# Optimization experiments

Hardware: AMD Instinct MI355X
Metric: run time of the kernel (lower is better)

Reference implementation:

```python
import jax, jax.numpy as jnp
import numpy as np
from jax.ops import segment_sum, segment_max

DIM = 64; EDGE_DIM = 6; ACTION_DIM = 6
N = 16384; E = 32768; G = 256; TPG = 12  # nodes, edges, graphs, torsions/graph


def setup_inputs() -> dict:
    key = jax.random.key(0)
    ks = jax.random.split(key, 16)
    d = DIM
    def lin(k, fo, fi):
        return (jax.random.normal(k, (fo, fi), jnp.float32) / np.sqrt(fi)).astype(jnp.float32)
    return {
        "x": jax.random.normal(ks[0], (N, 3), jnp.float32),
        "edge_attr": jax.random.normal(ks[1], (E, EDGE_DIM), jnp.float32),
        "edge_index": jax.random.randint(ks[2], (2, E), 0, N),
        "batch": (jnp.arange(N) // (N // G)).astype(jnp.int32),
        "nonring": jax.random.randint(ks[3], (G * TPG, 4), 0, N),
        "nrbidx": (jnp.arange(G * TPG) // TPG).astype(jnp.int32),
        "num_graphs": G,
        "torsion_size": TPG,
        "lin0_w": lin(ks[4], d, 3), "lin0_b": jnp.zeros((d,), jnp.float32),
        "e1_w": lin(ks[5], d, EDGE_DIM), "e1_b": jnp.zeros((d,), jnp.float32),
        "e2_w": lin(ks[6], d * d, d), "e2_b": jnp.zeros((d * d,), jnp.float32),
        "root_w": lin(ks[7], d, d), "conv_b": jnp.zeros((d,), jnp.float32),
        "gru_wih": lin(ks[8], 3 * d, d), "gru_whh": lin(ks[9], 3 * d, d),
        "gru_bih": jnp.zeros((3 * d,), jnp.float32), "gru_bhh": jnp.zeros((3 * d,), jnp.float32),
        "s2s_wih": lin(ks[10], 4 * d, 2 * d), "s2s_whh": lin(ks[11], 4 * d, d),
        "s2s_bih": jnp.zeros((4 * d,), jnp.float32), "s2s_bhh": jnp.zeros((4 * d,), jnp.float32),
        "mem_wih": lin(ks[12], 4 * d, 2 * d), "mem_whh": lin(ks[13], 4 * d, d),
        "mem_bih": jnp.zeros((4 * d,), jnp.float32), "mem_bhh": jnp.zeros((4 * d,), jnp.float32),
        "lin1_w": lin(ks[14], d, 5 * d), "lin1_b": jnp.zeros((d,), jnp.float32),
        "lin2_w": lin(ks[15], ACTION_DIM, d), "lin2_b": jnp.zeros((ACTION_DIM,), jnp.float32),
    }


def _lstm_step(xin, h, c, wih, whh, bih, bhh):
    g = xin @ wih.T + bih + h @ whh.T + bhh
    i, f, gg, o = jnp.split(g, 4, axis=-1)
    c = jax.nn.sigmoid(f) * c + jax.nn.sigmoid(i) * jnp.tanh(gg)
    h = jax.nn.sigmoid(o) * jnp.tanh(c)
    return h, c


def _model(x, edge_attr, lin0_w, lin0_b, e1_w, e1_b, e2_w, e2_b, root_w, conv_b,
           gru_wih, gru_whh, gru_bih, gru_bhh, s2s_wih, s2s_whh, s2s_bih, s2s_bhh,
           mem_wih, mem_whh, mem_bih, mem_bhh, lin1_w, lin1_b, lin2_w, lin2_b,
           edge_index, batch, nonring, nrbidx, num_graphs, torsion_size):
    d = lin0_w.shape[0]
    n = x.shape[0]
    out = jax.nn.relu(x @ lin0_w.T + lin0_b)           # [N, d]
    h = out                                            # GRU hidden
    src, dst = edge_index[0], edge_index[1]
    # edge-conditioned weights (fixed across the 6 iterations -> computed once)
    ew = (jax.nn.relu(edge_attr @ e1_w.T + e1_b) @ e2_w.T + e2_b).reshape(-1, d, d)  # [E, d, d]
    deg = jnp.clip(segment_sum(jnp.ones((src.shape[0],), out.dtype), dst, num_segments=n), 1.0)
    for _ in range(6):
        msg = jnp.einsum('ei,eio->eo', out[src], ew)   # per-edge matmul, [E, d]
        agg = segment_sum(msg, dst, num_segments=n) / deg[:, None]  # scatter-mean
        m = jax.nn.relu(agg + out @ root_w + conv_b)
        gi = m @ gru_wih.T + gru_bih
        gh = h @ gru_whh.T + gru_bhh
        r = jax.nn.sigmoid(gi[:, :d] + gh[:, :d])
        z = jax.nn.sigmoid(gi[:, d:2 * d] + gh[:, d:2 * d])
        nnew = jnp.tanh(gi[:, 2 * d:] + r * gh[:, 2 * d:])
        h = (1.0 - z) * nnew + z * h
        out = h
    # Set2Set pooling, 6 processing steps
    q_star = jnp.zeros((num_graphs, 2 * d), out.dtype)
    hs = jnp.zeros((num_graphs, d), out.dtype); cs = jnp.zeros_like(hs)
    for _ in range(6):
        hs, cs = _lstm_step(q_star, hs, cs, s2s_wih, s2s_whh, s2s_bih, s2s_bhh)
        e = jnp.sum(out * hs[batch], axis=-1)
        emax = segment_max(e, batch, num_segments=num_graphs)
        a = jnp.exp(e - emax[batch])
        a = a / segment_sum(a, batch, num_segments=num_graphs)[batch]
        r_ = segment_sum(a[:, None] * out, batch, num_segments=num_graphs)
        q_star = jnp.concatenate([hs, r_], axis=-1)
    # memory LSTM, single step from zero state
    hx = jnp.zeros((num_graphs, d), out.dtype); cx = jnp.zeros_like(hx)
    hx, cx = _lstm_step(q_star, hx, cx, mem_wih, mem_whh, mem_bih, mem_bhh)
    lstm_sel = hx[nrbidx]                                   # [T, d]
    node_sel = out[nonring.reshape(-1)].reshape(4, -1, d)   # faithful to .view(4,-1,dim)
    stacked = jnp.concatenate([lstm_sel[None], node_sel], axis=0)  # [5, T, d]
    feat = jnp.transpose(stacked, (2, 1, 0)).reshape(-1, 5 * d)    # faithful permute+reshape -> [T, 5d]
    o1 = jax.nn.relu(feat @ lin1_w.T + lin1_b)
    logits = o1 @ lin2_w.T + lin2_b                          # [T, action_dim]
    logit = logits.reshape(num_graphs, torsion_size, -1)     # uniform split + pad_sequence
    return logit, hx[None], cx[None]


def reference(x, edge_attr, edge_index, batch, nonring, nrbidx, num_graphs, torsion_size,
              lin0_w, lin0_b, e1_w, e1_b, e2_w, e2_b, root_w, conv_b,
              gru_wih, gru_whh, gru_bih, gru_bhh, s2s_wih, s2s_whh, s2s_bih, s2s_bhh,
              mem_wih, mem_whh, mem_bih, mem_bhh, lin1_w, lin1_b, lin2_w, lin2_b):
    return _model(x, edge_attr, lin0_w, lin0_b, e1_w, e1_b, e2_w, e2_b, root_w, conv_b,
                  gru_wih, gru_whh, gru_bih, gru_bhh, s2s_wih, s2s_whh, s2s_bih, s2s_bhh,
                  mem_wih, mem_whh, mem_bih, mem_bhh, lin1_w, lin1_b, lin2_w, lin2_b,
                  edge_index, batch, nonring, nrbidx, num_graphs, torsion_size)
```

## Files before the change

kernel.cpp:

```cpp
#include <hip/hip_runtime.h>

#define NNODE 16384
#define NEDGE 32768
#define NG    256
#define TPGx  12
#define TTOT  (NG * TPGx)
#define D     64

typedef _Float16 h8 __attribute__((ext_vector_type(8)));
typedef float    f4 __attribute__((ext_vector_type(4)));

static __device__ __forceinline__ float sigm(float x) { return 1.f / (1.f + __expf(-x)); }

static __device__ __forceinline__ f4 mfma16h(h8 a, h8 b, f4 c) {
  return __builtin_amdgcn_mfma_f32_16x16x32_f16(a, b, c, 0, 0, 0);
}

static __device__ __forceinline__ void gload_lds16(const void* g, void* l) {
  __builtin_amdgcn_global_load_lds(
      (const __attribute__((address_space(1))) unsigned int*)g,
      (__attribute__((address_space(3))) unsigned int*)l, 16, 0, 0);
}

#define WS_H      0
#define WS_AGG    4194304
#define WS_W2     8388608
#define WS_RT     8921088
#define WS_WHH    8929280
#define WS_WIH    8953856
#define WS_SWIH   8978432
#define WS_SWHH   9109504
#define WS_MWIH   9175040
#define WS_L1WF   9306112
#define WS_L2WF   9388032
#define WS_FB     9389568
#define WS_DEG    9398784
#define WS_HX     9464320
#define WS_NEED   9529856

struct Srcs { const void* p[23]; };

__device__ __constant__ const int kCum[24] = {
    0, 192, 256, 640, 704, 262848, 266944, 271040, 271104, 283392, 295680,
    295872, 296064, 328832, 345216, 345472, 345728, 378496, 378752, 379008,
    399488, 399552, 399936, 399942};

__global__ __launch_bounds__(256) void pack_kernel(Srcs S, char* __restrict__ ws) {
  int idx = blockIdx.x * 256 + threadIdx.x;
  if (idx >= 399942) return;
  int r = 0, base = 0;
#pragma unroll
  for (int k = 0; k < 23; k++)
    if (idx >= kCum[k]) { r = k; base = kCum[k]; }
  int li = idx - base;
  float v = ((const float*)S.p[r])[li];

  float*    fb   = (float*)(ws + WS_FB);
  _Float16* w2   = (_Float16*)(ws + WS_W2);
  _Float16* rtH  = (_Float16*)(ws + WS_RT);
  _Float16* whhH = (_Float16*)(ws + WS_WHH);
  _Float16* wihH = (_Float16*)(ws + WS_WIH);
  float*    swih = (float*)(ws + WS_SWIH);
  float*    swhh = (float*)(ws + WS_SWHH);
  float*    mwih = (float*)(ws + WS_MWIH);
  float*    l1w  = (float*)(ws + WS_L1WF);
  float*    l2w  = (float*)(ws + WS_L2WF);

  switch (r) {
    case 0: fb[li] = v; break;
    case 1: fb[192 + li] = v; break;
    case 2: fb[256 + li] = v; break;
    case 3: fb[640 + li] = v; break;
    case 4: {
      int i = li >> 12, o = (li >> 6) & 63, k = li & 63;
      w2[i * 4096 + (((k >> 3) * 64 + o) << 3) + (k & 7)] = (_Float16)v;
    } break;
    case 5: {
      int k = li >> 6, o = li & 63;
      w2[64 * 4096 + (((k >> 3) * 64 + o) << 3) + (k & 7)] = (_Float16)v;
    } break;
    case 6: {
      int i = li >> 6, o = li & 63;
      rtH[o * 64 + i] = (_Float16)v;
    } break;
    case 7: fb[704 + li] = v; break;
    case 8: wihH[li] = (_Float16)v; break;
    case 9: whhH[li] = (_Float16)v; break;
    case 10: fb[768 + li] = v; break;
    case 11: fb[960 + li] = v; break;
    case 12: swih[li] = v; break;
    case 13: swhh[li] = v; break;
    case 14: fb[1152 + li] = v; break;
    case 15: fb[1408 + li] = v; break;
    case 16: mwih[li] = v; break;
    case 17: fb[1664 + li] = v; break;
    case 18: fb[1920 + li] = v; break;
    case 19: l1w[li] = v; break;
    case 20: fb[2176 + li] = v; break;
    case 21: l2w[li] = v; break;
    case 22: fb[2240 + li] = v; break;
  }
}

__global__ __launch_bounds__(256) void init_kernel(
    const float* __restrict__ x, const float* __restrict__ fb,
    float* __restrict__ h) {
  int idx = blockIdx.x * 256 + threadIdx.x;
  int n = idx >> 6, o = idx & 63;
  float acc = fb[192 + o];
#pragma unroll
  for (int j = 0; j < 3; j++) acc += x[n * 3 + j] * fb[o * 3 + j];
  h[idx] = fmaxf(acc, 0.f);
}

__global__ __launch_bounds__(256) void deg_kernel(const int* __restrict__ edge_index,
                                                  float* __restrict__ deg) {
  int e = blockIdx.x * 256 + threadIdx.x;
  if (e < NEDGE) atomicAdd(&deg[edge_index[NEDGE + e]], 1.0f);
}

__global__ __launch_bounds__(256) void msg_kernel(
    const float* __restrict__ h, const float* __restrict__ ea,
    const float* __restrict__ fb, const _Float16* __restrict__ w2,
    const int* __restrict__ edge_index, float* __restrict__ agg) {
  __shared__ _Float16 sOut[64][72];
  __shared__ _Float16 sB[2][16384];
  const int tid = threadIdx.x;
  const int wave = tid >> 6, lane = tid & 63;
  const int m15 = lane & 15, quad = lane >> 4;
  const int eb = blockIdx.x * 64;
  {
    int r = tid >> 2, c0 = (tid & 3) * 16;
    int srcn = edge_index[eb + r];
#pragma unroll
    for (int c = c0; c < c0 + 16; c += 4) {
      float4 v = *(const float4*)&h[srcn * D + c];
      sOut[r][c]     = (_Float16)v.x;
      sOut[r][c + 1] = (_Float16)v.y;
      sOut[r][c + 2] = (_Float16)v.z;
      sOut[r][c + 3] = (_Float16)v.w;
    }
  }
  const int erow = wave * 16 + m15;
  const int e = eb + erow;
  float hid0[8], hid1[8];
  {
    float eav[6];
#pragma unroll
    for (int j = 0; j < 6; j++) eav[j] = ea[e * 6 + j];
#pragma unroll
    for (int j = 0; j < 8; j++) {
      int k0 = quad * 8 + j, k1 = 32 + quad * 8 + j;
      float a0 = fb[640 + k0], a1 = fb[640 + k1];
#pragma unroll
      for (int jj = 0; jj < 6; jj++) {
        a0 += eav[jj] * fb[256 + k0 * 6 + jj];
        a1 += eav[jj] * fb[256 + k1 * 6 + jj];
      }
      hid0[j] = fmaxf(a0, 0.f);
      hid1[j] = fmaxf(a1, 0.f);
    }
  }
  for (int c = wave; c < 32; c += 4)
    gload_lds16(w2 + c * 512 + lane * 8, &sB[0][c * 512]);
  __syncthreads();
  f4 zz = {0.f, 0.f, 0.f, 0.f};
  f4 acc0 = zz, acc1 = zz, acc2 = zz, acc3 = zz;
  for (int p = 0; p < 17; p++) {
    const int cur = p & 1;
    if (p < 16) {
      int nch = (p == 15) ? 8 : 32;
      const _Float16* src = w2 + (p + 1) * 4 * 4096;
      for (int c = wave; c < nch; c += 4)
        gload_lds16(src + c * 512 + lane * 8, &sB[cur ^ 1][c * 512]);
    }
    const int cnt = (p == 16) ? 1 : 4;
    for (int t = 0; t < cnt; t++) {
      const int i = p * 4 + t;
      h8 a0, a1;
      if (i < 64) {
        float os = (float)sOut[erow][i];
#pragma unroll
        for (int j = 0; j < 8; j++) {
          a0[j] = (_Float16)(os * hid0[j]);
          a1[j] = (_Float16)(os * hid1[j]);
        }
      } else {
#pragma unroll
        for (int j = 0; j < 8; j++) {
          a0[j] = sOut[erow][quad * 8 + j];
          a1[j] = sOut[erow][32 + quad * 8 + j];
        }
      }
      const _Float16* base = &sB[cur][t * 4096];
      const int q512 = quad * 512;
#pragma unroll
      for (int nt = 0; nt < 4; nt++) {
        int br8 = (nt * 16 + m15) * 8;
        h8 bh0 = *(const h8*)(base + q512 + br8);
        h8 bh1 = *(const h8*)(base + 2048 + q512 + br8);
        f4 a = (nt == 0) ? acc0 : (nt == 1) ? acc1 : (nt == 2) ? acc2 : acc3;
        a = mfma16h(a0, bh0, a);
        a = mfma16h(a1, bh1, a);
        if (nt == 0) acc0 = a; else if (nt == 1) acc1 = a; else if (nt == 2) acc2 = a; else acc3 = a;
      }
    }
    __syncthreads();
  }
#pragma unroll
  for (int reg = 0; reg < 4; reg++) {
    int ee = eb + wave * 16 + quad * 4 + reg;
    int dn = edge_index[NEDGE + ee];
    float* ap = agg + dn * D;
    atomicAdd(ap + m15,      acc0[reg]);
    atomicAdd(ap + 16 + m15, acc1[reg]);
    atomicAdd(ap + 32 + m15, acc2[reg]);
    atomicAdd(ap + 48 + m15, acc3[reg]);
  }
}

__global__ __launch_bounds__(256) void update_kernel(
    float* __restrict__ h, float* __restrict__ agg, const float* __restrict__ deg,
    const _Float16* __restrict__ rtH, const _Float16* __restrict__ whhH,
    const _Float16* __restrict__ wihH, const float* __restrict__ fb) {
  __shared__ float buf[64][68];
  const int tid = threadIdx.x;
  const int wave = tid >> 6, lane = tid & 63;
  const int m15 = lane & 15, quad = lane >> 4;
  const int nb = blockIdx.x * 64;
  {
    int r = tid >> 2, c0 = (tid & 3) * 16;
#pragma unroll
    for (int c = c0; c < c0 + 16; c += 4)
      *(float4*)&buf[r][c] = *(const float4*)&h[(nb + r) * D + c];
  }
  __syncthreads();
  const int mrow = wave * 16 + m15;
  h8 a0, a1;
#pragma unroll
  for (int j = 0; j < 8; j++) {
    a0[j] = (_Float16)buf[mrow][quad * 8 + j];
    a1[j] = (_Float16)buf[mrow][32 + quad * 8 + j];
  }
  f4 zz = {0.f, 0.f, 0.f, 0.f};
  f4 acc[16];
#pragma unroll
  for (int nt = 0; nt < 16; nt++) acc[nt] = zz;
#pragma unroll
  for (int nt = 0; nt < 16; nt++) {
    int nn = nt * 16 + m15;
    const _Float16* bp = (nt < 4) ? (rtH + nn * D) : (whhH + (nn - 64) * D);
    h8 bh0 = *(const h8*)(bp + quad * 8);
    h8 bh1 = *(const h8*)(bp + 32 + quad * 8);
    f4 a = acc[nt];
    a = mfma16h(a0, bh0, a);
    a = mfma16h(a1, bh1, a);
    acc[nt] = a;
  }
  __syncthreads();
#pragma unroll
  for (int nt = 0; nt < 4; nt++) {
#pragma unroll
    for (int reg = 0; reg < 4; reg++) {
      int nloc = wave * 16 + quad * 4 + reg;
      int o = nt * 16 + m15;
      float dg = fmaxf(deg[nb + nloc], 1.f);
      int aidx = (nb + nloc) * D + o;
      float v = acc[nt][reg] + agg[aidx] / dg + fb[704 + o];
      agg[aidx] = 0.f;
      buf[nloc][o] = fmaxf(v, 0.f);
    }
  }
  __syncthreads();
  h8 m0, m1;
#pragma unroll
  for (int j = 0; j < 8; j++) {
    m0[j] = (_Float16)buf[mrow][quad * 8 + j];
    m1[j] = (_Float16)buf[mrow][32 + quad * 8 + j];
  }
  f4 g2[12];
#pragma unroll
  for (int nt = 0; nt < 12; nt++) g2[nt] = zz;
#pragma unroll
  for (int nt = 0; nt < 12; nt++) {
    int nn = nt * 16 + m15;
    const _Float16* bp = wihH + nn * D;
    h8 bh0 = *(const h8*)(bp + quad * 8);
    h8 bh1 = *(const h8*)(bp + 32 + quad * 8);
    f4 a = g2[nt];
    a = mfma16h(m0, bh0, a);
    a = mfma16h(m1, bh1, a);
    g2[nt] = a;
  }
#pragma unroll
  for (int nt = 0; nt < 4; nt++) {
#pragma unroll
    for (int reg = 0; reg < 4; reg++) {
      int nloc = wave * 16 + quad * 4 + reg;
      int o = nt * 16 + m15;
      int gidx = (nb + nloc) * D + o;
      float gir = g2[nt][reg]      + fb[768 + o];
      float giz = g2[nt + 4][reg]  + fb[768 + 64 + o];
      float gin = g2[nt + 8][reg]  + fb[768 + 128 + o];
      float ghr = acc[nt + 4][reg]  + fb[960 + o];
      float ghz = acc[nt + 8][reg]  + fb[960 + 64 + o];
      float ghn = acc[nt + 12][reg] + fb[960 + 128 + o];
      float rr = sigm(gir + ghr);
      float zg = sigm(giz + ghz);
      float nnv = tanhf(gin + rr * ghn);
      float hv = h[gidx];
      h[gidx] = (1.f - zg) * nnv + zg * hv;
    }
  }
}

__global__ __launch_bounds__(256) void s2s_kernel(
    const float* __restrict__ h,
    const float* __restrict__ wih, const float* __restrict__ whhp,
    const float* __restrict__ mwih, const float* __restrict__ fb,
    float* __restrict__ hx_f32, float* __restrict__ dout) {
  __shared__ float outL[64][65];
  __shared__ float qs[128];
  __shared__ float hsv[64], csv[64], sg[256], sa[64];
  __shared__ float spart[4][64];
  const int t = threadIdx.x;
  const int g = blockIdx.x;
  for (int idx = t; idx < 64 * 64; idx += 256) outL[idx >> 6][idx & 63] = h[g * 4096 + idx];
  if (t < 128) qs[t] = 0.f;
  if (t < 64) { hsv[t] = 0.f; csv[t] = 0.f; }
  __syncthreads();
  for (int step = 0; step < 6; step++) {
    float acc = fb[1152 + t] + fb[1408 + t];
    const float* wr = wih + t * 128;
#pragma unroll 8
    for (int j = 0; j < 128; j++) acc += qs[j] * wr[j];
    const float* wr2 = whhp + t * 64;
#pragma unroll 8
    for (int j = 0; j < 64; j++) acc += hsv[j] * wr2[j];
    sg[t] = acc;
    __syncthreads();
    if (t < 64) {
      float cn = sigm(sg[64 + t]) * csv[t] + sigm(sg[t]) * tanhf(sg[128 + t]);
      csv[t] = cn;
      hsv[t] = sigm(sg[192 + t]) * tanhf(cn);
    }
    __syncthreads();
    if (t < 64) {
      float e = 0.f;
      for (int d2 = 0; d2 < 64; d2++) e += outL[t][d2] * hsv[d2];
      float mx = e;
      for (int off = 32; off > 0; off >>= 1) mx = fmaxf(mx, __shfl_xor(mx, off));
      float a = __expf(e - mx);
      float s = a;
      for (int off = 32; off > 0; off >>= 1) s += __shfl_xor(s, off);
      sa[t] = a / s;
    }
    __syncthreads();
    {
      int o = t & 63, part = t >> 6;
      float r = 0.f;
      for (int n2 = part * 16; n2 < part * 16 + 16; n2++) r += sa[n2] * outL[n2][o];
      spart[part][o] = r;
    }
    __syncthreads();
    if (t < 64) {
      qs[t] = hsv[t];
      qs[64 + t] = spart[0][t] + spart[1][t] + spart[2][t] + spart[3][t];
    }
    __syncthreads();
  }
  float acc = fb[1664 + t] + fb[1920 + t];
  const float* wr = mwih + t * 128;
#pragma unroll 8
  for (int j = 0; j < 128; j++) acc += qs[j] * wr[j];
  sg[t] = acc;
  __syncthreads();
  if (t < 64) {
    float cn = sigm(sg[t]) * tanhf(sg[128 + t]);
    float hn = sigm(sg[192 + t]) * tanhf(cn);
    hx_f32[g * 64 + t] = hn;
    dout[TTOT * 6 + g * 64 + t] = hn;
    dout[TTOT * 6 + NG * 64 + g * 64 + t] = cn;
  }
}

__global__ __launch_bounds__(64) void head_kernel(
    const float* __restrict__ h, const float* __restrict__ hx_f32,
    const int* __restrict__ nonring, const int* __restrict__ nrbidx,
    const float* __restrict__ l1w, const float* __restrict__ l2w,
    const float* __restrict__ fb, float* __restrict__ dout) {
  __shared__ float feat[320];
  __shared__ float so1[64];
  const int r = blockIdx.x;
  const int lane = threadIdx.x;
  const int blk = r % 48, di = r / 48;
  const int tt = blk * 64 + lane;
  feat[lane * 5] = hx_f32[nrbidx[tt] * 64 + di];
#pragma unroll
  for (int s = 1; s <= 4; s++)
    feat[lane * 5 + s] = h[nonring[(s - 1) * TTOT + tt] * 64 + di];
  __syncthreads();
  float acc = fb[2176 + lane];
  const float* wr = l1w + lane * 320;
#pragma unroll 8
  for (int c = 0; c < 320; c++) acc += feat[c] * wr[c];
  so1[lane] = fmaxf(acc, 0.f);
  __syncthreads();
  if (lane < 6) {
    float a2 = fb[2240 + lane];
    for (int j = 0; j < 64; j++) a2 += so1[j] * l2w[lane * 64 + j];
    dout[r * 6 + lane] = a2;
  }
}

extern "C" void kernel_launch(void* const* d_in, const int* in_sizes, int n_in,
                              void* d_out, int out_size, void* d_ws, size_t ws_size,
                              hipStream_t stream) {
  (void)in_sizes; (void)n_in; (void)out_size;
  const float* x         = (const float*)d_in[0];
  const float* edge_attr = (const float*)d_in[1];
  const int* edge_index  = (const int*)d_in[2];
  const int* nonring     = (const int*)d_in[4];
  const int* nrbidx      = (const int*)d_in[5];
  float* out = (float*)d_out;

  char* ws = (char*)d_ws;
  float*    h      = (float*)(ws + WS_H);
  float*    agg    = (float*)(ws + WS_AGG);
  _Float16* w2     = (_Float16*)(ws + WS_W2);
  _Float16* rtH    = (_Float16*)(ws + WS_RT);
  _Float16* whhH   = (_Float16*)(ws + WS_WHH);
  _Float16* wihH   = (_Float16*)(ws + WS_WIH);
  float*    swihF  = (float*)(ws + WS_SWIH);
  float*    swhhF  = (float*)(ws + WS_SWHH);
  float*    mwihF  = (float*)(ws + WS_MWIH);
  float*    l1wF   = (float*)(ws + WS_L1WF);
  float*    l2wF   = (float*)(ws + WS_L2WF);
  float*    fb     = (float*)(ws + WS_FB);
  float*    deg    = (float*)(ws + WS_DEG);
  float*    hx_f32 = (float*)(ws + WS_HX);
  if (ws_size < (size_t)WS_NEED) return;

  Srcs S;
  S.p[0] = d_in[8];   S.p[1] = d_in[9];   S.p[2] = d_in[10];  S.p[3] = d_in[11];
  S.p[4] = d_in[12];  S.p[5] = d_in[13];  S.p[6] = d_in[14];  S.p[7] = d_in[15];
  S.p[8] = d_in[16];  S.p[9] = d_in[17];  S.p[10] = d_in[18]; S.p[11] = d_in[19];
  S.p[12] = d_in[20]; S.p[13] = d_in[21]; S.p[14] = d_in[22]; S.p[15] = d_in[23];
  S.p[16] = d_in[24]; S.p[17] = d_in[26]; S.p[18] = d_in[27]; S.p[19] = d_in[28];
  S.p[20] = d_in[29]; S.p[21] = d_in[30]; S.p[22] = d_in[31];
  pack_kernel<<<(399942 + 255) / 256, 256, 0, stream>>>(S, ws);

  init_kernel<<<NNODE * D / 256, 256, 0, stream>>>(x, fb, h);
  hipMemsetAsync(deg, 0, NNODE * 4, stream);
  hipMemsetAsync(agg, 0, NNODE * D * 4, stream);
  deg_kernel<<<NEDGE / 256, 256, 0, stream>>>(edge_index, deg);

  for (int it = 0; it < 6; it++) {
    msg_kernel<<<NEDGE / 64, 256, 0, stream>>>(h, edge_attr, fb, w2, edge_index, agg);
    update_kernel<<<NNODE / 64, 256, 0, stream>>>(h, agg, deg, rtH, whhH, wihH, fb);
  }

  s2s_kernel<<<NG, 256, 0, stream>>>(h, swihF, swhhF, mwihF, fb, hx_f32, out);
  head_kernel<<<TTOT, 64, 0, stream>>>(h, hx_f32, nonring, nrbidx, l1wF, l2wF, fb, out);
}
```

Measured before the change: 540.0 us.

## Double msg_kernel edge tile, halve weight staging, transpose s2s/head weights

msg_kernel now handles 128 edges per block instead of 64. Each wave runs two 16-edge row tiles against the same B fragment loaded from LDS, which halves global-to-LDS traffic for the 64x64x64 edge-network weight per edge. The A operand is now built with packed fp16 vector multiplies on a precomputed fp16 hidden vector instead of a scalar fp32 loop. Separately, the s2s LSTM and head lin1 weights are packed transposed so that threads read them with coalesced loads. In exchange, msg_kernel uses more accumulator registers, launches half as many blocks, and rounds the hidden activations to fp16 before multiplying, which slightly changes numerics.

```diff
diff --git a/kernel.cpp b/kernel.cpp
--- a/kernel.cpp
+++ b/kernel.cpp
@@ -16,6 +16,11 @@
   return __builtin_amdgcn_mfma_f32_16x16x32_f16(a, b, c, 0, 0, 0);
 }
 
+static __device__ __forceinline__ h8 splat16(_Float16 x) {
+  h8 v = {x, x, x, x, x, x, x, x};
+  return v;
+}
+
 static __device__ __forceinline__ void gload_lds16(const void* g, void* l) {
   __builtin_amdgcn_global_load_lds(
       (const __attribute__((address_space(1))) unsigned int*)g,
@@ -28,10 +33,10 @@
 #define WS_RT     8921088
 #define WS_WHH    8929280
 #define WS_WIH    8953856
-#define WS_SWIH   8978432
-#define WS_SWHH   9109504
-#define WS_MWIH   9175040
-#define WS_L1WF   9306112
+#define WS_SWIHT  8978432
+#define WS_SWHHT  9109504
+#define WS_MWIHT  9175040
+#define WS_L1WT   9306112
 #define WS_L2WF   9388032
 #define WS_FB     9389568
 #define WS_DEG    9398784
@@ -55,16 +60,16 @@
   int li = idx - base;
   float v = ((const float*)S.p[r])[li];
 
-  float*    fb   = (float*)(ws + WS_FB);
-  _Float16* w2   = (_Float16*)(ws + WS_W2);
-  _Float16* rtH  = (_Float16*)(ws + WS_RT);
-  _Float16* whhH = (_Float16*)(ws + WS_WHH);
-  _Float16* wihH = (_Float16*)(ws + WS_WIH);
-  float*    swih = (float*)(ws + WS_SWIH);
-  float*    swhh = (float*)(ws + WS_SWHH);
-  float*    mwih = (float*)(ws + WS_MWIH);
-  float*    l1w  = (float*)(ws + WS_L1WF);
-  float*    l2w  = (float*)(ws + WS_L2WF);
+  float*    fb    = (float*)(ws + WS_FB);
+  _Float16* w2    = (_Float16*)(ws + WS_W2);
+  _Float16* rtH   = (_Float16*)(ws + WS_RT);
+  _Float16* whhH  = (_Float16*)(ws + WS_WHH);
+  _Float16* wihH  = (_Float16*)(ws + WS_WIH);
+  float*    swihT = (float*)(ws + WS_SWIHT);
+  float*    swhhT = (float*)(ws + WS_SWHHT);
+  float*    mwihT = (float*)(ws + WS_MWIHT);
+  float*    l1wT  = (float*)(ws + WS_L1WT);
+  float*    l2w   = (float*)(ws + WS_L2WF);
 
   switch (r) {
     case 0: fb[li] = v; break;
@@ -88,14 +93,14 @@
     case 9: whhH[li] = (_Float16)v; break;
     case 10: fb[768 + li] = v; break;
     case 11: fb[960 + li] = v; break;
-    case 12: swih[li] = v; break;
-    case 13: swhh[li] = v; break;
+    case 12: swihT[(li & 127) * 256 + (li >> 7)] = v; break;
+    case 13: swhhT[(li & 63) * 256 + (li >> 6)] = v; break;
     case 14: fb[1152 + li] = v; break;
     case 15: fb[1408 + li] = v; break;
-    case 16: mwih[li] = v; break;
+    case 16: mwihT[(li & 127) * 256 + (li >> 7)] = v; break;
     case 17: fb[1664 + li] = v; break;
     case 18: fb[1920 + li] = v; break;
-    case 19: l1w[li] = v; break;
+    case 19: l1wT[(li % 320) * 64 + (li / 320)] = v; break;
     case 20: fb[2176 + li] = v; break;
     case 21: l2w[li] = v; break;
     case 22: fb[2240 + li] = v; break;
@@ -123,17 +128,17 @@
     const float* __restrict__ h, const float* __restrict__ ea,
     const float* __restrict__ fb, const _Float16* __restrict__ w2,
     const int* __restrict__ edge_index, float* __restrict__ agg) {
-  __shared__ _Float16 sOut[64][72];
-  __shared__ _Float16 sB[2][16384];
+  __shared__ _Float16 sOut[128][72];
+  __shared__ _Float16 sB[2][8192];
   const int tid = threadIdx.x;
   const int wave = tid >> 6, lane = tid & 63;
   const int m15 = lane & 15, quad = lane >> 4;
-  const int eb = blockIdx.x * 64;
+  const int eb = blockIdx.x * 128;
   {
-    int r = tid >> 2, c0 = (tid & 3) * 16;
+    int r = tid >> 1, c0 = (tid & 1) * 32;
     int srcn = edge_index[eb + r];
 #pragma unroll
-    for (int c = c0; c < c0 + 16; c += 4) {
+    for (int c = c0; c < c0 + 32; c += 4) {
       float4 v = *(const float4*)&h[srcn * D + c];
       sOut[r][c]     = (_Float16)v.x;
       sOut[r][c + 1] = (_Float16)v.y;
@@ -141,56 +146,60 @@
       sOut[r][c + 3] = (_Float16)v.w;
     }
   }
-  const int erow = wave * 16 + m15;
-  const int e = eb + erow;
-  float hid0[8], hid1[8];
+  const int erow1 = wave * 16 + m15;
+  const int erow2 = 64 + erow1;
+  const int e1 = eb + erow1, e2 = eb + erow2;
+  h8 hidA0, hidA1, hidB0, hidB1;
   {
-    float eav[6];
-#pragma unroll
-    for (int j = 0; j < 6; j++) eav[j] = ea[e * 6 + j];
+    float eav1[6], eav2[6];
+#pragma unroll
+    for (int j = 0; j < 6; j++) { eav1[j] = ea[e1 * 6 + j]; eav2[j] = ea[e2 * 6 + j]; }
 #pragma unroll
     for (int j = 0; j < 8; j++) {
       int k0 = quad * 8 + j, k1 = 32 + quad * 8 + j;
-      float a0 = fb[640 + k0], a1 = fb[640 + k1];
+      float a01 = fb[640 + k0], a11 = fb[640 + k1];
+      float a02 = a01, a12 = a11;
 #pragma unroll
       for (int jj = 0; jj < 6; jj++) {
-        a0 += eav[jj] * fb[256 + k0 * 6 + jj];
-        a1 += eav[jj] * fb[256 + k1 * 6 + jj];
+        float w0 = fb[256 + k0 * 6 + jj], w1 = fb[256 + k1 * 6 + jj];
+        a01 += eav1[jj] * w0; a11 += eav1[jj] * w1;
+        a02 += eav2[jj] * w0; a12 += eav2[jj] * w1;
       }
-      hid0[j] = fmaxf(a0, 0.f);
-      hid1[j] = fmaxf(a1, 0.f);
-    }
-  }
-  for (int c = wave; c < 32; c += 4)
+      hidA0[j] = (_Float16)fmaxf(a01, 0.f);
+      hidA1[j] = (_Float16)fmaxf(a11, 0.f);
+      hidB0[j] = (_Float16)fmaxf(a02, 0.f);
+      hidB1[j] = (_Float16)fmaxf(a12, 0.f);
+    }
+  }
+  for (int c = wave; c < 16; c += 4)
     gload_lds16(w2 + c * 512 + lane * 8, &sB[0][c * 512]);
   __syncthreads();
   f4 zz = {0.f, 0.f, 0.f, 0.f};
-  f4 acc0 = zz, acc1 = zz, acc2 = zz, acc3 = zz;
-  for (int p = 0; p < 17; p++) {
+  f4 accA[4], accB[4];
+#pragma unroll
+  for (int nt = 0; nt < 4; nt++) { accA[nt] = zz; accB[nt] = zz; }
+  for (int p = 0; p < 33; p++) {
     const int cur = p & 1;
-    if (p < 16) {
-      int nch = (p == 15) ? 8 : 32;
-      const _Float16* src = w2 + (p + 1) * 4 * 4096;
+    if (p < 32) {
+      int nch = (p == 31) ? 8 : 16;
+      const _Float16* src = w2 + (p + 1) * 8192;
       for (int c = wave; c < nch; c += 4)
         gload_lds16(src + c * 512 + lane * 8, &sB[cur ^ 1][c * 512]);
     }
-    const int cnt = (p == 16) ? 1 : 4;
+    const int cnt = (p == 32) ? 1 : 2;
     for (int t = 0; t < cnt; t++) {
-      const int i = p * 4 + t;
-      h8 a0, a1;
+      const int i = p * 2 + t;
+      h8 a10, a11, a20, a21;
       if (i < 64) {
-        float os = (float)sOut[erow][i];
-#pragma unroll
-        for (int j = 0; j < 8; j++) {
-          a0[j] = (_Float16)(os * hid0[j]);
-          a1[j] = (_Float16)(os * hid1[j]);
-        }
+        h8 o1 = splat16(sOut[erow1][i]);
+        h8 o2 = splat16(sOut[erow2][i]);
+        a10 = hidA0 * o1; a11 = hidA1 * o1;
+        a20 = hidB0 * o2; a21 = hidB1 * o2;
       } else {
-#pragma unroll
-        for (int j = 0; j < 8; j++) {
-          a0[j] = sOut[erow][quad * 8 + j];
-          a1[j] = sOut[erow][32 + quad * 8 + j];
-        }
+        a10 = *(const h8*)&sOut[erow1][quad * 8];
+        a11 = *(const h8*)&sOut[erow1][32 + quad * 8];
+        a20 = *(const h8*)&sOut[erow2][quad * 8];
+        a21 = *(const h8*)&sOut[erow2][32 + quad * 8];
       }
       const _Float16* base = &sB[cur][t * 4096];
       const int q512 = quad * 512;
@@ -199,23 +208,27 @@
         int br8 = (nt * 16 + m15) * 8;
         h8 bh0 = *(const h8*)(base + q512 + br8);
         h8 bh1 = *(const h8*)(base + 2048 + q512 + br8);
-        f4 a = (nt == 0) ? acc0 : (nt == 1) ? acc1 : (nt == 2) ? acc2 : acc3;
-        a = mfma16h(a0, bh0, a);
-        a = mfma16h(a1, bh1, a);
-        if (nt == 0) acc0 = a; else if (nt == 1) acc1 = a; else if (nt == 2) acc2 = a; else acc3 = a;
+        accA[nt] = mfma16h(a10, bh0, accA[nt]);
+        accA[nt] = mfma16h(a11, bh1, accA[nt]);
+        accB[nt] = mfma16h(a20, bh0, accB[nt]);
+        accB[nt] = mfma16h(a21, bh1, accB[nt]);
       }
     }
     __syncthreads();
   }
 #pragma unroll
   for (int reg = 0; reg < 4; reg++) {
-    int ee = eb + wave * 16 + quad * 4 + reg;
-    int dn = edge_index[NEDGE + ee];
-    float* ap = agg + dn * D;
-    atomicAdd(ap + m15,      acc0[reg]);
-    atomicAdd(ap + 16 + m15, acc1[reg]);
-    atomicAdd(ap + 32 + m15, acc2[reg]);
-    atomicAdd(ap + 48 + m15, acc3[reg]);
+    int r1 = eb + wave * 16 + quad * 4 + reg;
+    int r2 = r1 + 64;
+    int dn1 = edge_index[NEDGE + r1];
+    int dn2 = edge_index[NEDGE + r2];
+    float* ap1 = agg + dn1 * D;
+    float* ap2 = agg + dn2 * D;
+#pragma unroll
+    for (int nt = 0; nt < 4; nt++) {
+      atomicAdd(ap1 + nt * 16 + m15, accA[nt][reg]);
+      atomicAdd(ap2 + nt * 16 + m15, accB[nt][reg]);
+    }
   }
 }
 
@@ -316,8 +329,8 @@
 
 __global__ __launch_bounds__(256) void s2s_kernel(
     const float* __restrict__ h,
-    const float* __restrict__ wih, const float* __restrict__ whhp,
-    const float* __restrict__ mwih, const float* __restrict__ fb,
+    const float* __restrict__ wihT, const float* __restrict__ whhT,
+    const float* __restrict__ mwihT, const float* __restrict__ fb,
     float* __restrict__ hx_f32, float* __restrict__ dout) {
   __shared__ float outL[64][65];
   __shared__ float qs[128];
@@ -331,12 +344,10 @@
   __syncthreads();
   for (int step = 0; step < 6; step++) {
     float acc = fb[1152 + t] + fb[1408 + t];
-    const float* wr = wih + t * 128;
 #pragma unroll 8
-    for (int j = 0; j < 128; j++) acc += qs[j] * wr[j];
-    const float* wr2 = whhp + t * 64;
+    for (int j = 0; j < 128; j++) acc += qs[j] * wihT[j * 256 + t];
 #pragma unroll 8
-    for (int j = 0; j < 64; j++) acc += hsv[j] * wr2[j];
+    for (int j = 0; j < 64; j++) acc += hsv[j] * whhT[j * 256 + t];
     sg[t] = acc;
     __syncthreads();
     if (t < 64) {
@@ -370,9 +381,8 @@
     __syncthreads();
   }
   float acc = fb[1664 + t] + fb[1920 + t];
-  const float* wr = mwih + t * 128;
 #pragma unroll 8
-  for (int j = 0; j < 128; j++) acc += qs[j] * wr[j];
+  for (int j = 0; j < 128; j++) acc += qs[j] * mwihT[j * 256 + t];
   sg[t] = acc;
   __syncthreads();
   if (t < 64) {
@@ -387,7 +397,7 @@
 __global__ __launch_bounds__(64) void head_kernel(
     const float* __restrict__ h, const float* __restrict__ hx_f32,
     const int* __restrict__ nonring, const int* __restrict__ nrbidx,
-    const float* __restrict__ l1w, const float* __restrict__ l2w,
+    const float* __restrict__ l1wT, const float* __restrict__ l2w,
     const float* __restrict__ fb, float* __restrict__ dout) {
   __shared__ float feat[320];
   __shared__ float so1[64];
@@ -401,9 +411,8 @@
     feat[lane * 5 + s] = h[nonring[(s - 1) * TTOT + tt] * 64 + di];
   __syncthreads();
   float acc = fb[2176 + lane];
-  const float* wr = l1w + lane * 320;
 #pragma unroll 8
-  for (int c = 0; c < 320; c++) acc += feat[c] * wr[c];
+  for (int c = 0; c < 320; c++) acc += feat[c] * l1wT[c * 64 + lane];
   so1[lane] = fmaxf(acc, 0.f);
   __syncthreads();
   if (lane < 6) {
@@ -431,10 +440,10 @@
   _Float16* rtH    = (_Float16*)(ws + WS_RT);
   _Float16* whhH   = (_Float16*)(ws + WS_WHH);
   _Float16* wihH   = (_Float16*)(ws + WS_WIH);
-  float*    swihF  = (float*)(ws + WS_SWIH);
-  float*    swhhF  = (float*)(ws + WS_SWHH);
-  float*    mwihF  = (float*)(ws + WS_MWIH);
-  float*    l1wF   = (float*)(ws + WS_L1WF);
+  float*    swihT  = (float*)(ws + WS_SWIHT);
+  float*    swhhT  = (float*)(ws + WS_SWHHT);
+  float*    mwihT  = (float*)(ws + WS_MWIHT);
+  float*    l1wT   = (float*)(ws + WS_L1WT);
   float*    l2wF   = (float*)(ws + WS_L2WF);
   float*    fb     = (float*)(ws + WS_FB);
   float*    deg    = (float*)(ws + WS_DEG);
@@ -456,10 +465,10 @@
   deg_kernel<<<NEDGE / 256, 256, 0, stream>>>(edge_index, deg);
 
   for (int it = 0; it < 6; it++) {
-    msg_kernel<<<NEDGE / 64, 256, 0, stream>>>(h, edge_attr, fb, w2, edge_index, agg);
+    msg_kernel<<<NEDGE / 128, 256, 0, stream>>>(h, edge_attr, fb, w2, edge_index, agg);
     update_kernel<<<NNODE / 64, 256, 0, stream>>>(h, agg, deg, rtH, whhH, wihH, fb);
   }
 
-  s2s_kernel<<<NG, 256, 0, stream>>>(h, swihF, swhhF, mwihF, fb, hx_f32, out);
-  head_kernel<<<TTOT, 64, 0, stream>>>(h, hx_f32, nonring, nrbidx, l1wF, l2wF, fb, out);
-}
+  s2s_kernel<<<NG, 256, 0, stream>>>(h, swihT, swhhT, mwihT, fb, hx_f32, out);
+  head_kernel<<<TTOT, 64, 0, stream>>>(h, hx_f32, nonring, nrbidx, l1wT, l2wF, fb, out);
+}
```

Measured after the change: 530.3 us. Within noise of the previous version (-1.8%).
